# Optimization experiments

Hardware: AMD Instinct MI355X
Metric: run time of the kernel (lower is better)

## Reference

```python
import jax, jax.numpy as jnp
import numpy as np

B, T, IN, H, NC = 256, 512, 64, 512, 64
H2 = H // 2


def setup_inputs() -> dict:
    key = jax.random.key(0)
    ks = jax.random.split(key, 13)
    s = 0.05
    return {
        "x": jax.random.normal(ks[0], (B, T, IN), jnp.float32),
        # layer 0 LSTM weights (PyTorch layout: [4H, in], gate order i,f,g,o)
        "w_ih0": jax.random.normal(ks[1], (4 * H, IN), jnp.float32) * s,
        "w_hh0": jax.random.normal(ks[2], (4 * H, H), jnp.float32) * s,
        "b_ih0": jax.random.normal(ks[3], (4 * H,), jnp.float32) * s,
        "b_hh0": jax.random.normal(ks[4], (4 * H,), jnp.float32) * s,
        # layer 1 LSTM weights
        "w_ih1": jax.random.normal(ks[5], (4 * H, H), jnp.float32) * s,
        "w_hh1": jax.random.normal(ks[6], (4 * H, H), jnp.float32) * s,
        "b_ih1": jax.random.normal(ks[7], (4 * H,), jnp.float32) * s,
        "b_hh1": jax.random.normal(ks[8], (4 * H,), jnp.float32) * s,
        # classifier head
        "w1": jax.random.normal(ks[9], (H2, H), jnp.float32) * s,
        "b1": jax.random.normal(ks[10], (H2,), jnp.float32) * s,
        "w2": jax.random.normal(ks[11], (NC, H2), jnp.float32) * s,
        "b2": jax.random.normal(ks[12], (NC,), jnp.float32) * s,
    }


def _lstm_layer(x, w_ih, w_hh, b_ih, b_hh):
    # x: [B, T, D_in] -> hidden sequence [B, T, H]
    b, t, _ = x.shape
    h_dim = w_hh.shape[1]
    # precompute input projection for all time steps: [B, T, 4H]
    gx = jnp.einsum('btd,gd->btg', x, w_ih) + b_ih + b_hh

    def step(carry, g_t):
        h, c = carry
        gates = g_t + h @ w_hh.T  # [B, 4H]
        i, f, g, o = jnp.split(gates, 4, axis=-1)
        i = jax.nn.sigmoid(i)
        f = jax.nn.sigmoid(f)
        g = jnp.tanh(g)
        o = jax.nn.sigmoid(o)
        c_new = f * c + i * g
        h_new = o * jnp.tanh(c_new)
        return (h_new, c_new), h_new

    h0 = jnp.zeros((b, h_dim), x.dtype)
    c0 = jnp.zeros((b, h_dim), x.dtype)
    (_, _), hs = jax.lax.scan(step, (h0, c0), jnp.swapaxes(gx, 0, 1))
    return jnp.swapaxes(hs, 0, 1)  # [B, T, H]


def reference(x, w_ih0, w_hh0, b_ih0, b_hh0, w_ih1, w_hh1, b_ih1, b_hh1, w1, b1, w2, b2):
    # 2-layer LSTM (eval mode: inter-layer dropout disabled)
    out = _lstm_layer(x, w_ih0, w_hh0, b_ih0, b_hh0)
    out = _lstm_layer(out, w_ih1, w_hh1, b_ih1, b_hh1)
    feat = out[:, -1, :]  # last time step hidden state [B, H]
    # classifier: Linear -> ReLU -> (Dropout off in eval) -> Linear
    hmid = jax.nn.relu(feat @ w1.T + b1)
    logits = hmid @ w2.T + b2
    return logits
```

## Files before the change

### kernel.cpp

```cpp
#include <hip/hip_runtime.h>
#include <stdint.h>

#define B_  256
#define T_  512
#define IN_ 64
#define H_  512
#define G4_ 2048
#define NC_ 64
#define H2_ 256

typedef _Float16 f16;
typedef __attribute__((ext_vector_type(4))) _Float16 f16x4;
typedef __attribute__((ext_vector_type(4))) float    f32x4;
typedef __attribute__((ext_vector_type(4))) unsigned int u32x4;

__device__ __forceinline__ float sigf(float x) {
  return __builtin_amdgcn_rcpf(1.0f + __expf(-x));
}
__device__ __forceinline__ float tanh_fast(float x) {
  x = fminf(fmaxf(x, -15.f), 15.f);
  const float e = __expf(2.f * x);
  return (e - 1.f) * __builtin_amdgcn_rcpf(e + 1.f);
}

__device__ __forceinline__ void store_u32_l3(void* p, unsigned v) {
  asm volatile("global_store_dword %0, %1, off sc0 sc1" :: "v"(p), "v"(v) : "memory");
}
__device__ __forceinline__ void store_f32_l3(void* p, float v) {
  asm volatile("global_store_dword %0, %1, off sc0 sc1" :: "v"(p), "v"(v) : "memory");
}
__device__ __forceinline__ unsigned load_u32_l3(const void* p) {
  unsigned r;
  asm volatile("global_load_dword %0, %1, off sc0 sc1" : "=v"(r) : "v"(p) : "memory");
  return r;
}
__device__ __forceinline__ float load_f32_l3(const void* p) {
  float r;
  asm volatile("global_load_dword %0, %1, off sc0 sc1" : "=v"(r) : "v"(p) : "memory");
  return r;
}
__device__ __forceinline__ u32x4 load_u32x4_l3(const void* p) {
  u32x4 r;
  asm volatile("global_load_dwordx4 %0, %1, off sc0 sc1" : "=v"(r) : "v"(p) : "memory");
  return r;
}
__device__ __forceinline__ void wait_vm0() {
  asm volatile("s_waitcnt vmcnt(0)" ::: "memory");
}

__global__ void cvt_f32_f16(const float* __restrict__ s, f16* __restrict__ d, int n) {
  int i = blockIdx.x * blockDim.x + threadIdx.x;
  int st = gridDim.x * blockDim.x;
  for (; i < n; i += st) d[i] = (f16)s[i];
}

__global__ void bias_comb(const float* __restrict__ a, const float* __restrict__ b,
                          float* __restrict__ d, int n) {
  int i = blockIdx.x * blockDim.x + threadIdx.x;
  if (i < n) d[i] = a[i] + b[i];
}

__global__ __launch_bounds__(512, 2) void fused_g(
    const f16* __restrict__ x16,
    const f16* __restrict__ wih0,
    const f16* __restrict__ whh0,
    const f16* __restrict__ wih1,
    const f16* __restrict__ whh1,
    const float* __restrict__ bias0,
    const float* __restrict__ bias1,
    f16* __restrict__ h0seq,
    float* __restrict__ gxring,
    f16* __restrict__ hbuf1,
    unsigned* __restrict__ flags) {
  __shared__ __align__(16) unsigned char smem[36352];
  const int bid = blockIdx.x;
  const int tid = threadIdx.x;
  const int lane = tid & 63, wv = tid >> 6;
  const int l15 = lane & 15, hi = lane >> 4;

  if (bid < 128) {
    const int grp = bid >> 3, sl = bid & 7;
    f16 (*xt)[72]   = (f16(*)[72])smem;
    f16 (*ht)[532]  = (f16(*)[532])(smem + 2304);
    float (*gl)[260] = (float(*)[260])(smem + 2304 + 17024);

    int gidx[2]; f16x4 bhh[2][32]; f16x4 bih[2][4]; float bv[2];
#pragma unroll
    for (int nt = 0; nt < 2; ++nt) {
      const int lg = (wv * 2 + nt) * 16 + l15;
      const int grow = (lg >> 6) * H_ + sl * 64 + (lg & 63);
      gidx[nt] = grow; bv[nt] = bias0[grow];
      const f16* wp = whh0 + (size_t)grow * H_;
#pragma unroll
      for (int ks = 0; ks < 32; ++ks) bhh[nt][ks] = *(const f16x4*)(wp + ks * 16 + 4 * hi);
      const f16* wq = wih0 + (size_t)grow * IN_;
#pragma unroll
      for (int ks = 0; ks < 4; ++ks) bih[nt][ks] = *(const f16x4*)(wq + ks * 16 + 4 * hi);
    }

    const int bl = tid >> 5;
    const int j0 = (tid & 31) * 2;
    float c0 = 0.f, c1 = 0.f;
    const int hrow = tid >> 5, hcol = (tid & 31) * 16;

    for (int t = 0; t < T_; ++t) {
      if (tid < 128) {
        const f16* xs = x16 + ((size_t)(grp * 16 + (tid >> 3)) * T_ + t) * IN_ + (tid & 7) * 8;
        *(uint4*)&xt[tid >> 3][(tid & 7) * 8] = *(const uint4*)xs;
      }
      if (t != 0) {
        const unsigned* pp = flags + (size_t)(grp * 8 + (lane & 7)) * 16;
        const unsigned want = (unsigned)t;
        for (;;) {
          unsigned v = load_u32_l3(pp); wait_vm0();
          if (__all((int)(v >= want))) break;
          __builtin_amdgcn_s_sleep(1);
        }
        const f16* hs = h0seq + ((size_t)(t - 1) * B_ + grp * 16 + hrow) * H_ + hcol;
        u32x4 r0 = load_u32x4_l3(hs);
        u32x4 r1 = load_u32x4_l3(hs + 8);
        wait_vm0();
        __builtin_amdgcn_sched_barrier(0);
        *(u32x4*)&ht[hrow][hcol]     = r0;
        *(u32x4*)&ht[hrow][hcol + 8] = r1;
      } else {
        u32x4 z = {0u, 0u, 0u, 0u};
        *(u32x4*)&ht[hrow][hcol]     = z;
        *(u32x4*)&ht[hrow][hcol + 8] = z;
      }
      __syncthreads();

      f32x4 acc[2];
#pragma unroll
      for (int nt = 0; nt < 2; ++nt) { acc[nt][0] = bv[nt]; acc[nt][1] = bv[nt]; acc[nt][2] = bv[nt]; acc[nt][3] = bv[nt]; }
#pragma unroll
      for (int ks = 0; ks < 4; ++ks) {
        const f16x4 a = *(const f16x4*)&xt[l15][ks * 16 + 4 * hi];
        acc[0] = __builtin_amdgcn_mfma_f32_16x16x16f16(a, bih[0][ks], acc[0], 0, 0, 0);
        acc[1] = __builtin_amdgcn_mfma_f32_16x16x16f16(a, bih[1][ks], acc[1], 0, 0, 0);
      }
#pragma unroll
      for (int ks = 0; ks < 32; ++ks) {
        const f16x4 a = *(const f16x4*)&ht[l15][ks * 16 + 4 * hi];
        acc[0] = __builtin_amdgcn_mfma_f32_16x16x16f16(a, bhh[0][ks], acc[0], 0, 0, 0);
        acc[1] = __builtin_amdgcn_mfma_f32_16x16x16f16(a, bhh[1][ks], acc[1], 0, 0, 0);
      }
#pragma unroll
      for (int nt = 0; nt < 2; ++nt) {
        const int col = (wv * 2 + nt) * 16 + l15;
#pragma unroll
        for (int r = 0; r < 4; ++r) gl[4 * hi + r][col] = acc[nt][r];
      }
      __syncthreads();

      const float gi = gl[bl][j0],        gi1 = gl[bl][j0 + 1];
      const float gf = gl[bl][64 + j0],   gf1 = gl[bl][64 + j0 + 1];
      const float gg = gl[bl][128 + j0],  gg1 = gl[bl][128 + j0 + 1];
      const float go = gl[bl][192 + j0],  go1 = gl[bl][192 + j0 + 1];
      c0 = sigf(gf) * c0 + sigf(gi) * tanh_fast(gg);
      c1 = sigf(gf1) * c1 + sigf(gi1) * tanh_fast(gg1);
      const f16 h0h = (f16)(sigf(go) * tanh_fast(c0));
      const f16 h1h = (f16)(sigf(go1) * tanh_fast(c1));
      unsigned hp = ((unsigned)__builtin_bit_cast(unsigned short, h1h) << 16)
                  |  (unsigned)__builtin_bit_cast(unsigned short, h0h);
      store_u32_l3(h0seq + ((size_t)t * B_ + grp * 16 + bl) * H_ + sl * 64 + j0, hp);
      wait_vm0();
      __syncthreads();
      if (tid == 0) store_u32_l3(flags + (size_t)(grp * 8 + sl) * 16, (unsigned)(t + 1));
    }

  } else if (bid < 192) {
    const int bg = (bid - 128) >> 3, slB = (bid - 128) & 7;
    f16 (*ht)[532] = (f16(*)[532])smem;

    int gidx[2]; f16x4 bih[2][32]; float bv[2];
#pragma unroll
    for (int nt = 0; nt < 2; ++nt) {
      const int grow = slB * 256 + (wv * 2 + nt) * 16 + l15;
      gidx[nt] = grow; bv[nt] = bias1[grow];
      const f16* wp = wih1 + (size_t)grow * H_;
#pragma unroll
      for (int ks = 0; ks < 32; ++ks) bih[nt][ks] = *(const f16x4*)(wp + ks * 16 + 4 * hi);
    }
    const int hrow = tid >> 4, hcol = (tid & 15) * 32;

    for (int t = 0; t < T_; ++t) {
      {
        const bool isC = (lane >= 16 && lane < 24);
        const unsigned wantC = (t >= 8) ? (unsigned)(t - 7) : 0u;
        const int slot = isC ? (192 + bg * 8 + (lane - 16)) : (bg * 16 + (lane & 15));
        const unsigned want = isC ? wantC : (unsigned)(t + 1);
        const unsigned* pp = flags + (size_t)slot * 16;
        for (;;) {
          unsigned v = load_u32_l3(pp); wait_vm0();
          if (__all((int)(v >= want))) break;
          __builtin_amdgcn_s_sleep(1);
        }
      }
      {
        const f16* hs = h0seq + ((size_t)t * B_ + bg * 32 + hrow) * H_ + hcol;
        u32x4 r0 = load_u32x4_l3(hs);
        u32x4 r1 = load_u32x4_l3(hs + 8);
        u32x4 r2 = load_u32x4_l3(hs + 16);
        u32x4 r3 = load_u32x4_l3(hs + 24);
        wait_vm0();
        __builtin_amdgcn_sched_barrier(0);
        *(u32x4*)&ht[hrow][hcol]      = r0;
        *(u32x4*)&ht[hrow][hcol + 8]  = r1;
        *(u32x4*)&ht[hrow][hcol + 16] = r2;
        *(u32x4*)&ht[hrow][hcol + 24] = r3;
      }
      __syncthreads();

      f32x4 acc[2][2] = {};
#pragma unroll
      for (int ks = 0; ks < 32; ++ks) {
        const f16x4 a0 = *(const f16x4*)&ht[l15][ks * 16 + 4 * hi];
        const f16x4 a1 = *(const f16x4*)&ht[16 + l15][ks * 16 + 4 * hi];
        acc[0][0] = __builtin_amdgcn_mfma_f32_16x16x16f16(a0, bih[0][ks], acc[0][0], 0, 0, 0);
        acc[0][1] = __builtin_amdgcn_mfma_f32_16x16x16f16(a0, bih[1][ks], acc[0][1], 0, 0, 0);
        acc[1][0] = __builtin_amdgcn_mfma_f32_16x16x16f16(a1, bih[0][ks], acc[1][0], 0, 0, 0);
        acc[1][1] = __builtin_amdgcn_mfma_f32_16x16x16f16(a1, bih[1][ks], acc[1][1], 0, 0, 0);
      }
      float* gp = gxring + (size_t)(t & 7) * B_ * G4_;
#pragma unroll
      for (int mt = 0; mt < 2; ++mt)
#pragma unroll
        for (int nt = 0; nt < 2; ++nt)
#pragma unroll
          for (int r = 0; r < 4; ++r)
            store_f32_l3(gp + (size_t)(bg * 32 + mt * 16 + 4 * hi + r) * G4_ + gidx[nt],
                         acc[mt][nt][r] + bv[nt]);
      wait_vm0();
      __syncthreads();
      if (tid == 0) store_u32_l3(flags + (size_t)(128 + bg * 8 + slB) * 16, (unsigned)(t + 1));
    }

  } else {
    const int bg = (bid - 192) >> 3, slC = (bid - 192) & 7;
    f16 (*ht)[532]   = (f16(*)[532])smem;
    float (*gl)[260] = (float(*)[260])smem;

    int gidx[2]; f16x4 bhh[2][32];
#pragma unroll
    for (int nt = 0; nt < 2; ++nt) {
      const int lg = (wv * 2 + nt) * 16 + l15;
      const int grow = (lg >> 6) * H_ + slC * 64 + (lg & 63);
      gidx[nt] = grow;
      const f16* wp = whh1 + (size_t)grow * H_;
#pragma unroll
      for (int ks = 0; ks < 32; ++ks) bhh[nt][ks] = *(const f16x4*)(wp + ks * 16 + 4 * hi);
    }
    const int r0row = tid >> 5;
    const int j0 = (tid & 31) * 2;
    float c00 = 0.f, c01 = 0.f, c10 = 0.f, c11 = 0.f;
    const int hrow = tid >> 4, hcol = (tid & 15) * 32;

    for (int t = 0; t < T_; ++t) {
      {
        const bool isOwn = (lane >= 8 && lane < 16);
        const unsigned wantOwn = (t >= 1) ? (unsigned)t : 0u;
        const int slot = isOwn ? (192 + bg * 8 + (lane - 8)) : (128 + bg * 8 + (lane & 7));
        const unsigned want = isOwn ? wantOwn : (unsigned)(t + 1);
        const unsigned* pp = flags + (size_t)slot * 16;
        for (;;) {
          unsigned v = load_u32_l3(pp); wait_vm0();
          if (__all((int)(v >= want))) break;
          __builtin_amdgcn_s_sleep(1);
        }
      }
      float gxv[2][2][4];
      const float* gp = gxring + (size_t)(t & 7) * B_ * G4_;
#pragma unroll
      for (int mt = 0; mt < 2; ++mt)
#pragma unroll
        for (int nt = 0; nt < 2; ++nt)
#pragma unroll
          for (int r = 0; r < 4; ++r)
            gxv[mt][nt][r] = load_f32_l3(gp + (size_t)(bg * 32 + mt * 16 + 4 * hi + r) * G4_ + gidx[nt]);
      if (t != 0) {
        const f16* hs = hbuf1 + ((size_t)((t - 1) & 1) * B_ + bg * 32 + hrow) * H_ + hcol;
        u32x4 r0 = load_u32x4_l3(hs);
        u32x4 r1 = load_u32x4_l3(hs + 8);
        u32x4 r2 = load_u32x4_l3(hs + 16);
        u32x4 r3 = load_u32x4_l3(hs + 24);
        wait_vm0();
        __builtin_amdgcn_sched_barrier(0);
        *(u32x4*)&ht[hrow][hcol]      = r0;
        *(u32x4*)&ht[hrow][hcol + 8]  = r1;
        *(u32x4*)&ht[hrow][hcol + 16] = r2;
        *(u32x4*)&ht[hrow][hcol + 24] = r3;
      } else {
        wait_vm0();
        u32x4 z = {0u, 0u, 0u, 0u};
        *(u32x4*)&ht[hrow][hcol]      = z;
        *(u32x4*)&ht[hrow][hcol + 8]  = z;
        *(u32x4*)&ht[hrow][hcol + 16] = z;
        *(u32x4*)&ht[hrow][hcol + 24] = z;
      }
      __syncthreads();

      f32x4 acc[2][2];
#pragma unroll
      for (int mt = 0; mt < 2; ++mt)
#pragma unroll
        for (int nt = 0; nt < 2; ++nt)
#pragma unroll
          for (int r = 0; r < 4; ++r) acc[mt][nt][r] = gxv[mt][nt][r];
#pragma unroll
      for (int ks = 0; ks < 32; ++ks) {
        const f16x4 a0 = *(const f16x4*)&ht[l15][ks * 16 + 4 * hi];
        const f16x4 a1 = *(const f16x4*)&ht[16 + l15][ks * 16 + 4 * hi];
        acc[0][0] = __builtin_amdgcn_mfma_f32_16x16x16f16(a0, bhh[0][ks], acc[0][0], 0, 0, 0);
        acc[0][1] = __builtin_amdgcn_mfma_f32_16x16x16f16(a0, bhh[1][ks], acc[0][1], 0, 0, 0);
        acc[1][0] = __builtin_amdgcn_mfma_f32_16x16x16f16(a1, bhh[0][ks], acc[1][0], 0, 0, 0);
        acc[1][1] = __builtin_amdgcn_mfma_f32_16x16x16f16(a1, bhh[1][ks], acc[1][1], 0, 0, 0);
      }
      __syncthreads();
#pragma unroll
      for (int mt = 0; mt < 2; ++mt)
#pragma unroll
        for (int nt = 0; nt < 2; ++nt) {
          const int col = (wv * 2 + nt) * 16 + l15;
#pragma unroll
          for (int r = 0; r < 4; ++r) gl[mt * 16 + 4 * hi + r][col] = acc[mt][nt][r];
        }
      __syncthreads();

      const int cur = t & 1;
#pragma unroll
      for (int half = 0; half < 2; ++half) {
        const int row = r0row + half * 16;
        const float gi = gl[row][j0],        gi1 = gl[row][j0 + 1];
        const float gf = gl[row][64 + j0],   gf1 = gl[row][64 + j0 + 1];
        const float gg = gl[row][128 + j0],  gg1 = gl[row][128 + j0 + 1];
        const float go = gl[row][192 + j0],  go1 = gl[row][192 + j0 + 1];
        float& ca = half ? c10 : c00;
        float& cb = half ? c11 : c01;
        ca = sigf(gf) * ca + sigf(gi) * tanh_fast(gg);
        cb = sigf(gf1) * cb + sigf(gi1) * tanh_fast(gg1);
        const f16 ha = (f16)(sigf(go) * tanh_fast(ca));
        const f16 hb = (f16)(sigf(go1) * tanh_fast(cb));
        unsigned hp = ((unsigned)__builtin_bit_cast(unsigned short, hb) << 16)
                    |  (unsigned)__builtin_bit_cast(unsigned short, ha);
        store_u32_l3(hbuf1 + ((size_t)cur * B_ + bg * 32 + row) * H_ + slC * 64 + j0, hp);
      }
      wait_vm0();
      __syncthreads();
      if (tid == 0) store_u32_l3(flags + (size_t)(192 + bg * 8 + slC) * 16, (unsigned)(t + 1));
    }
  }
}

__global__ void head_g(const f16* __restrict__ h1, const float* __restrict__ w1,
                       const float* __restrict__ b1, const float* __restrict__ w2,
                       const float* __restrict__ b2, float* __restrict__ out) {
  __shared__ float ft[512];
  __shared__ float hm[256];
  const int b = blockIdx.x, tid = threadIdx.x;
  ft[tid * 2]     = (float)h1[(size_t)b * H_ + tid * 2];
  ft[tid * 2 + 1] = (float)h1[(size_t)b * H_ + tid * 2 + 1];
  __syncthreads();
  {
    float d = b1[tid];
    const float* wr = w1 + (size_t)tid * H_;
#pragma unroll 8
    for (int k = 0; k < H_; ++k) d += ft[k] * wr[k];
    hm[tid] = fmaxf(d, 0.f);
  }
  __syncthreads();
  if (tid < NC_) {
    float d = b2[tid];
    const float* wr = w2 + (size_t)tid * H2_;
#pragma unroll 8
    for (int k = 0; k < H2_; ++k) d += hm[k] * wr[k];
    out[(size_t)b * NC_ + tid] = d;
  }
}

extern "C" void kernel_launch(void* const* d_in, const int* in_sizes, int n_in,
                              void* d_out, int out_size, void* d_ws, size_t ws_size,
                              hipStream_t stream) {
  const float* x     = (const float*)d_in[0];
  const float* w_ih0 = (const float*)d_in[1];
  const float* w_hh0 = (const float*)d_in[2];
  const float* b_ih0 = (const float*)d_in[3];
  const float* b_hh0 = (const float*)d_in[4];
  const float* w_ih1 = (const float*)d_in[5];
  const float* w_hh1 = (const float*)d_in[6];
  const float* b_ih1 = (const float*)d_in[7];
  const float* b_hh1 = (const float*)d_in[8];
  const float* w1    = (const float*)d_in[9];
  const float* b1    = (const float*)d_in[10];
  const float* w2    = (const float*)d_in[11];
  const float* b2    = (const float*)d_in[12];
  float* out = (float*)d_out;

  char* p = (char*)d_ws;
  auto alloc = [&](size_t bytes) { char* r = p; p += (bytes + 255) & ~(size_t)255; return r; };
  f16*   h0seq  = (f16*)alloc((size_t)T_ * B_ * H_ * 2);
  float* gxring = (float*)alloc((size_t)8 * B_ * G4_ * 4);
  f16*   hbuf1  = (f16*)alloc((size_t)2 * B_ * H_ * 2);
  f16*   x16    = (f16*)alloc((size_t)B_ * T_ * IN_ * 2);
  f16*   wih0h  = (f16*)alloc((size_t)G4_ * IN_ * 2);
  f16*   whh0h  = (f16*)alloc((size_t)G4_ * H_ * 2);
  f16*   wih1h  = (f16*)alloc((size_t)G4_ * H_ * 2);
  f16*   whh1h  = (f16*)alloc((size_t)G4_ * H_ * 2);
  float* bias0c = (float*)alloc(G4_ * 4);
  float* bias1c = (float*)alloc(G4_ * 4);
  unsigned* flags = (unsigned*)alloc(256 * 64);

  hipMemsetAsync(flags, 0, 256 * 64, stream);
  cvt_f32_f16<<<2048, 256, 0, stream>>>(x, x16, B_ * T_ * IN_);
  cvt_f32_f16<<<512, 256, 0, stream>>>(w_ih0, wih0h, G4_ * IN_);
  cvt_f32_f16<<<2048, 256, 0, stream>>>(w_hh0, whh0h, G4_ * H_);
  cvt_f32_f16<<<2048, 256, 0, stream>>>(w_ih1, wih1h, G4_ * H_);
  cvt_f32_f16<<<2048, 256, 0, stream>>>(w_hh1, whh1h, G4_ * H_);
  bias_comb<<<8, 256, 0, stream>>>(b_ih0, b_hh0, bias0c, G4_);
  bias_comb<<<8, 256, 0, stream>>>(b_ih1, b_hh1, bias1c, G4_);

  fused_g<<<256, 512, 0, stream>>>(x16, wih0h, whh0h, wih1h, whh1h,
                                   bias0c, bias1c, h0seq, gxring, hbuf1, flags);
  head_g<<<B_, 256, 0, stream>>>(hbuf1 + (size_t)B_ * H_, w1, b1, w2, b2, out);
}
```

Before: 3.309 ms.

## Fuse layer-1 input projection into recurrent blocks, drop gx ring buffer

Measured after the change: 3.518 ms. 6.3% more time.

```diff
diff --git a/kernel.cpp b/kernel.cpp
--- a/kernel.cpp
+++ b/kernel.cpp
@@ -26,16 +26,8 @@
 __device__ __forceinline__ void store_u32_l3(void* p, unsigned v) {
   asm volatile("global_store_dword %0, %1, off sc0 sc1" :: "v"(p), "v"(v) : "memory");
 }
-__device__ __forceinline__ void store_f32_l3(void* p, float v) {
-  asm volatile("global_store_dword %0, %1, off sc0 sc1" :: "v"(p), "v"(v) : "memory");
-}
 __device__ __forceinline__ unsigned load_u32_l3(const void* p) {
   unsigned r;
-  asm volatile("global_load_dword %0, %1, off sc0 sc1" : "=v"(r) : "v"(p) : "memory");
-  return r;
-}
-__device__ __forceinline__ float load_f32_l3(const void* p) {
-  float r;
   asm volatile("global_load_dword %0, %1, off sc0 sc1" : "=v"(r) : "v"(p) : "memory");
   return r;
 }
@@ -69,10 +61,9 @@
     const float* __restrict__ bias0,
     const float* __restrict__ bias1,
     f16* __restrict__ h0seq,
-    float* __restrict__ gxring,
     f16* __restrict__ hbuf1,
     unsigned* __restrict__ flags) {
-  __shared__ __align__(16) unsigned char smem[36352];
+  __shared__ __align__(16) unsigned char smem[50688];
   const int bid = blockIdx.x;
   const int tid = threadIdx.x;
   const int lane = tid & 63, wv = tid >> 6;
@@ -169,27 +160,36 @@
       if (tid == 0) store_u32_l3(flags + (size_t)(grp * 8 + sl) * 16, (unsigned)(t + 1));
     }
 
-  } else if (bid < 192) {
-    const int bg = (bid - 128) >> 3, slB = (bid - 128) & 7;
-    f16 (*ht)[532] = (f16(*)[532])smem;
-
-    int gidx[2]; f16x4 bih[2][32]; float bv[2];
+  } else {
+    const int grp = (bid - 128) >> 3, sl = (bid - 128) & 7;
+    f16 (*ht0)[532]  = (f16(*)[532])smem;
+    f16 (*ht1)[532]  = (f16(*)[532])(smem + 17024);
+    float (*gl)[260] = (float(*)[260])(smem + 34048);
+
+    int gidx[2]; f16x4 bih[2][32]; f16x4 bhh[2][32]; float bv[2];
 #pragma unroll
     for (int nt = 0; nt < 2; ++nt) {
-      const int grow = slB * 256 + (wv * 2 + nt) * 16 + l15;
+      const int lg = (wv * 2 + nt) * 16 + l15;
+      const int grow = (lg >> 6) * H_ + sl * 64 + (lg & 63);
       gidx[nt] = grow; bv[nt] = bias1[grow];
       const f16* wp = wih1 + (size_t)grow * H_;
 #pragma unroll
       for (int ks = 0; ks < 32; ++ks) bih[nt][ks] = *(const f16x4*)(wp + ks * 16 + 4 * hi);
+      const f16* wq = whh1 + (size_t)grow * H_;
+#pragma unroll
+      for (int ks = 0; ks < 32; ++ks) bhh[nt][ks] = *(const f16x4*)(wq + ks * 16 + 4 * hi);
     }
-    const int hrow = tid >> 4, hcol = (tid & 15) * 32;
+
+    const int bl = tid >> 5;
+    const int j0 = (tid & 31) * 2;
+    float c0 = 0.f, c1 = 0.f;
+    const int hrow = tid >> 5, hcol = (tid & 31) * 16;
 
     for (int t = 0; t < T_; ++t) {
       {
-        const bool isC = (lane >= 16 && lane < 24);
-        const unsigned wantC = (t >= 8) ? (unsigned)(t - 7) : 0u;
-        const int slot = isC ? (192 + bg * 8 + (lane - 16)) : (bg * 16 + (lane & 15));
-        const unsigned want = isC ? wantC : (unsigned)(t + 1);
+        const bool isOwn = (lane >= 8 && lane < 16);
+        const int slot = isOwn ? (128 + grp * 8 + (lane - 8)) : (grp * 8 + (lane & 7));
+        const unsigned want = isOwn ? (unsigned)t : (unsigned)(t + 1);
         const unsigned* pp = flags + (size_t)slot * 16;
         for (;;) {
           unsigned v = load_u32_l3(pp); wait_vm0();
@@ -198,156 +198,66 @@
         }
       }
       {
-        const f16* hs = h0seq + ((size_t)t * B_ + bg * 32 + hrow) * H_ + hcol;
-        u32x4 r0 = load_u32x4_l3(hs);
-        u32x4 r1 = load_u32x4_l3(hs + 8);
-        u32x4 r2 = load_u32x4_l3(hs + 16);
-        u32x4 r3 = load_u32x4_l3(hs + 24);
-        wait_vm0();
-        __builtin_amdgcn_sched_barrier(0);
-        *(u32x4*)&ht[hrow][hcol]      = r0;
-        *(u32x4*)&ht[hrow][hcol + 8]  = r1;
-        *(u32x4*)&ht[hrow][hcol + 16] = r2;
-        *(u32x4*)&ht[hrow][hcol + 24] = r3;
-      }
-      __syncthreads();
-
-      f32x4 acc[2][2] = {};
+        const f16* hs0 = h0seq + ((size_t)t * B_ + grp * 16 + hrow) * H_ + hcol;
+        u32x4 r0 = load_u32x4_l3(hs0);
+        u32x4 r1 = load_u32x4_l3(hs0 + 8);
+        if (t != 0) {
+          const f16* hs1 = hbuf1 + ((size_t)((t - 1) & 1) * B_ + grp * 16 + hrow) * H_ + hcol;
+          u32x4 r2 = load_u32x4_l3(hs1);
+          u32x4 r3 = load_u32x4_l3(hs1 + 8);
+          wait_vm0();
+          __builtin_amdgcn_sched_barrier(0);
+          *(u32x4*)&ht1[hrow][hcol]     = r2;
+          *(u32x4*)&ht1[hrow][hcol + 8] = r3;
+        } else {
+          wait_vm0();
+          __builtin_amdgcn_sched_barrier(0);
+          u32x4 z = {0u, 0u, 0u, 0u};
+          *(u32x4*)&ht1[hrow][hcol]     = z;
+          *(u32x4*)&ht1[hrow][hcol + 8] = z;
+        }
+        *(u32x4*)&ht0[hrow][hcol]     = r0;
+        *(u32x4*)&ht0[hrow][hcol + 8] = r1;
+      }
+      __syncthreads();
+
+      f32x4 acc[2];
+#pragma unroll
+      for (int nt = 0; nt < 2; ++nt) { acc[nt][0] = bv[nt]; acc[nt][1] = bv[nt]; acc[nt][2] = bv[nt]; acc[nt][3] = bv[nt]; }
 #pragma unroll
       for (int ks = 0; ks < 32; ++ks) {
-        const f16x4 a0 = *(const f16x4*)&ht[l15][ks * 16 + 4 * hi];
-        const f16x4 a1 = *(const f16x4*)&ht[16 + l15][ks * 16 + 4 * hi];
-        acc[0][0] = __builtin_amdgcn_mfma_f32_16x16x16f16(a0, bih[0][ks], acc[0][0], 0, 0, 0);
-        acc[0][1] = __builtin_amdgcn_mfma_f32_16x16x16f16(a0, bih[1][ks], acc[0][1], 0, 0, 0);
-        acc[1][0] = __builtin_amdgcn_mfma_f32_16x16x16f16(a1, bih[0][ks], acc[1][0], 0, 0, 0);
-        acc[1][1] = __builtin_amdgcn_mfma_f32_16x16x16f16(a1, bih[1][ks], acc[1][1], 0, 0, 0);
-      }
-      float* gp = gxring + (size_t)(t & 7) * B_ * G4_;
-#pragma unroll
-      for (int mt = 0; mt < 2; ++mt)
-#pragma unroll
-        for (int nt = 0; nt < 2; ++nt)
-#pragma unroll
-          for (int r = 0; r < 4; ++r)
-            store_f32_l3(gp + (size_t)(bg * 32 + mt * 16 + 4 * hi + r) * G4_ + gidx[nt],
-                         acc[mt][nt][r] + bv[nt]);
+        const f16x4 a0 = *(const f16x4*)&ht0[l15][ks * 16 + 4 * hi];
+        acc[0] = __builtin_amdgcn_mfma_f32_16x16x16f16(a0, bih[0][ks], acc[0], 0, 0, 0);
+        acc[1] = __builtin_amdgcn_mfma_f32_16x16x16f16(a0, bih[1][ks], acc[1], 0, 0, 0);
+      }
+#pragma unroll
+      for (int ks = 0; ks < 32; ++ks) {
+        const f16x4 a1 = *(const f16x4*)&ht1[l15][ks * 16 + 4 * hi];
+        acc[0] = __builtin_amdgcn_mfma_f32_16x16x16f16(a1, bhh[0][ks], acc[0], 0, 0, 0);
+        acc[1] = __builtin_amdgcn_mfma_f32_16x16x16f16(a1, bhh[1][ks], acc[1], 0, 0, 0);
+      }
+#pragma unroll
+      for (int nt = 0; nt < 2; ++nt) {
+        const int col = (wv * 2 + nt) * 16 + l15;
+#pragma unroll
+        for (int r = 0; r < 4; ++r) gl[4 * hi + r][col] = acc[nt][r];
+      }
+      __syncthreads();
+
+      const float gi = gl[bl][j0],        gi1 = gl[bl][j0 + 1];
+      const float gf = gl[bl][64 + j0],   gf1 = gl[bl][64 + j0 + 1];
+      const float gg = gl[bl][128 + j0],  gg1 = gl[bl][128 + j0 + 1];
+      const float go = gl[bl][192 + j0],  go1 = gl[bl][192 + j0 + 1];
+      c0 = sigf(gf) * c0 + sigf(gi) * tanh_fast(gg);
+      c1 = sigf(gf1) * c1 + sigf(gi1) * tanh_fast(gg1);
+      const f16 ha = (f16)(sigf(go) * tanh_fast(c0));
+      const f16 hb = (f16)(sigf(go1) * tanh_fast(c1));
+      unsigned hp = ((unsigned)__builtin_bit_cast(unsigned short, hb) << 16)
+                  |  (unsigned)__builtin_bit_cast(unsigned short, ha);
+      store_u32_l3(hbuf1 + ((size_t)(t & 1) * B_ + grp * 16 + bl) * H_ + sl * 64 + j0, hp);
       wait_vm0();
       __syncthreads();
-      if (tid == 0) store_u32_l3(flags + (size_t)(128 + bg * 8 + slB) * 16, (unsigned)(t + 1));
-    }
-
-  } else {
-    const int bg = (bid - 192) >> 3, slC = (bid - 192) & 7;
-    f16 (*ht)[532]   = (f16(*)[532])smem;
-    float (*gl)[260] = (float(*)[260])smem;
-
-    int gidx[2]; f16x4 bhh[2][32];
-#pragma unroll
-    for (int nt = 0; nt < 2; ++nt) {
-      const int lg = (wv * 2 + nt) * 16 + l15;
-      const int grow = (lg >> 6) * H_ + slC * 64 + (lg & 63);
-      gidx[nt] = grow;
-      const f16* wp = whh1 + (size_t)grow * H_;
-#pragma unroll
-      for (int ks = 0; ks < 32; ++ks) bhh[nt][ks] = *(const f16x4*)(wp + ks * 16 + 4 * hi);
-    }
-    const int r0row = tid >> 5;
-    const int j0 = (tid & 31) * 2;
-    float c00 = 0.f, c01 = 0.f, c10 = 0.f, c11 = 0.f;
-    const int hrow = tid >> 4, hcol = (tid & 15) * 32;
-
-    for (int t = 0; t < T_; ++t) {
-      {
-        const bool isOwn = (lane >= 8 && lane < 16);
-        const unsigned wantOwn = (t >= 1) ? (unsigned)t : 0u;
-        const int slot = isOwn ? (192 + bg * 8 + (lane - 8)) : (128 + bg * 8 + (lane & 7));
-        const unsigned want = isOwn ? wantOwn : (unsigned)(t + 1);
-        const unsigned* pp = flags + (size_t)slot * 16;
-        for (;;) {
-          unsigned v = load_u32_l3(pp); wait_vm0();
-          if (__all((int)(v >= want))) break;
-          __builtin_amdgcn_s_sleep(1);
-        }
-      }
-      float gxv[2][2][4];
-      const float* gp = gxring + (size_t)(t & 7) * B_ * G4_;
-#pragma unroll
-      for (int mt = 0; mt < 2; ++mt)
-#pragma unroll
-        for (int nt = 0; nt < 2; ++nt)
-#pragma unroll
-          for (int r = 0; r < 4; ++r)
-            gxv[mt][nt][r] = load_f32_l3(gp + (size_t)(bg * 32 + mt * 16 + 4 * hi + r) * G4_ + gidx[nt]);
-      if (t != 0) {
-        const f16* hs = hbuf1 + ((size_t)((t - 1) & 1) * B_ + bg * 32 + hrow) * H_ + hcol;
-        u32x4 r0 = load_u32x4_l3(hs);
-        u32x4 r1 = load_u32x4_l3(hs + 8);
-        u32x4 r2 = load_u32x4_l3(hs + 16);
-        u32x4 r3 = load_u32x4_l3(hs + 24);
-        wait_vm0();
-        __builtin_amdgcn_sched_barrier(0);
-        *(u32x4*)&ht[hrow][hcol]      = r0;
-        *(u32x4*)&ht[hrow][hcol + 8]  = r1;
-        *(u32x4*)&ht[hrow][hcol + 16] = r2;
-        *(u32x4*)&ht[hrow][hcol + 24] = r3;
-      } else {
-        wait_vm0();
-        u32x4 z = {0u, 0u, 0u, 0u};
-        *(u32x4*)&ht[hrow][hcol]      = z;
-        *(u32x4*)&ht[hrow][hcol + 8]  = z;
-        *(u32x4*)&ht[hrow][hcol + 16] = z;
-        *(u32x4*)&ht[hrow][hcol + 24] = z;
-      }
-      __syncthreads();
-
-      f32x4 acc[2][2];
-#pragma unroll
-      for (int mt = 0; mt < 2; ++mt)
-#pragma unroll
-        for (int nt = 0; nt < 2; ++nt)
-#pragma unroll
-          for (int r = 0; r < 4; ++r) acc[mt][nt][r] = gxv[mt][nt][r];
-#pragma unroll
-      for (int ks = 0; ks < 32; ++ks) {
-        const f16x4 a0 = *(const f16x4*)&ht[l15][ks * 16 + 4 * hi];
-        const f16x4 a1 = *(const f16x4*)&ht[16 + l15][ks * 16 + 4 * hi];
-        acc[0][0] = __builtin_amdgcn_mfma_f32_16x16x16f16(a0, bhh[0][ks], acc[0][0], 0, 0, 0);
-        acc[0][1] = __builtin_amdgcn_mfma_f32_16x16x16f16(a0, bhh[1][ks], acc[0][1], 0, 0, 0);
-        acc[1][0] = __builtin_amdgcn_mfma_f32_16x16x16f16(a1, bhh[0][ks], acc[1][0], 0, 0, 0);
-        acc[1][1] = __builtin_amdgcn_mfma_f32_16x16x16f16(a1, bhh[1][ks], acc[1][1], 0, 0, 0);
-      }
-      __syncthreads();
-#pragma unroll
-      for (int mt = 0; mt < 2; ++mt)
-#pragma unroll
-        for (int nt = 0; nt < 2; ++nt) {
-          const int col = (wv * 2 + nt) * 16 + l15;
-#pragma unroll
-          for (int r = 0; r < 4; ++r) gl[mt * 16 + 4 * hi + r][col] = acc[mt][nt][r];
-        }
-      __syncthreads();
-
-      const int cur = t & 1;
-#pragma unroll
-      for (int half = 0; half < 2; ++half) {
-        const int row = r0row + half * 16;
-        const float gi = gl[row][j0],        gi1 = gl[row][j0 + 1];
-        const float gf = gl[row][64 + j0],   gf1 = gl[row][64 + j0 + 1];
-        const float gg = gl[row][128 + j0],  gg1 = gl[row][128 + j0 + 1];
-        const float go = gl[row][192 + j0],  go1 = gl[row][192 + j0 + 1];
-        float& ca = half ? c10 : c00;
-        float& cb = half ? c11 : c01;
-        ca = sigf(gf) * ca + sigf(gi) * tanh_fast(gg);
-        cb = sigf(gf1) * cb + sigf(gi1) * tanh_fast(gg1);
-        const f16 ha = (f16)(sigf(go) * tanh_fast(ca));
-        const f16 hb = (f16)(sigf(go1) * tanh_fast(cb));
-        unsigned hp = ((unsigned)__builtin_bit_cast(unsigned short, hb) << 16)
-                    |  (unsigned)__builtin_bit_cast(unsigned short, ha);
-        store_u32_l3(hbuf1 + ((size_t)cur * B_ + bg * 32 + row) * H_ + slC * 64 + j0, hp);
-      }
-      wait_vm0();
-      __syncthreads();
-      if (tid == 0) store_u32_l3(flags + (size_t)(192 + bg * 8 + slC) * 16, (unsigned)(t + 1));
+      if (tid == 0) store_u32_l3(flags + (size_t)(128 + grp * 8 + sl) * 16, (unsigned)(t + 1));
     }
   }
 }
@@ -399,7 +309,6 @@
   char* p = (char*)d_ws;
   auto alloc = [&](size_t bytes) { char* r = p; p += (bytes + 255) & ~(size_t)255; return r; };
   f16*   h0seq  = (f16*)alloc((size_t)T_ * B_ * H_ * 2);
-  float* gxring = (float*)alloc((size_t)8 * B_ * G4_ * 4);
   f16*   hbuf1  = (f16*)alloc((size_t)2 * B_ * H_ * 2);
   f16*   x16    = (f16*)alloc((size_t)B_ * T_ * IN_ * 2);
   f16*   wih0h  = (f16*)alloc((size_t)G4_ * IN_ * 2);
@@ -420,6 +329,6 @@
   bias_comb<<<8, 256, 0, stream>>>(b_ih1, b_hh1, bias1c, G4_);
 
   fused_g<<<256, 512, 0, stream>>>(x16, wih0h, whh0h, wih1h, whh1h,
-                                   bias0c, bias1c, h0seq, gxring, hbuf1, flags);
+                                   bias0c, bias1c, h0seq, hbuf1, flags);
   head_g<<<B_, 256, 0, stream>>>(hbuf1 + (size_t)B_ * H_, w1, b1, w2, b2, out);
 }
```

## Store layer-1 input-gate ring in fp16, transposed, with deeper ring

Applied to the files above, without the earlier changes.

Result: slower. 3.480 ms (+5.2%).

```diff
diff --git a/kernel.cpp b/kernel.cpp
--- a/kernel.cpp
+++ b/kernel.cpp
@@ -12,6 +12,7 @@
 typedef _Float16 f16;
 typedef __attribute__((ext_vector_type(4))) _Float16 f16x4;
 typedef __attribute__((ext_vector_type(4))) float    f32x4;
+typedef __attribute__((ext_vector_type(2))) unsigned int u32x2;
 typedef __attribute__((ext_vector_type(4))) unsigned int u32x4;
 
 __device__ __forceinline__ float sigf(float x) {
@@ -22,21 +23,31 @@
   const float e = __expf(2.f * x);
   return (e - 1.f) * __builtin_amdgcn_rcpf(e + 1.f);
 }
+__device__ __forceinline__ unsigned pack2(float a, float b) {
+  return ((unsigned)__builtin_bit_cast(unsigned short, (f16)b) << 16)
+       |  (unsigned)__builtin_bit_cast(unsigned short, (f16)a);
+}
+__device__ __forceinline__ float unpk_lo(unsigned u) {
+  return (float)__builtin_bit_cast(f16, (unsigned short)(u & 0xffffu));
+}
+__device__ __forceinline__ float unpk_hi(unsigned u) {
+  return (float)__builtin_bit_cast(f16, (unsigned short)(u >> 16));
+}
 
 __device__ __forceinline__ void store_u32_l3(void* p, unsigned v) {
   asm volatile("global_store_dword %0, %1, off sc0 sc1" :: "v"(p), "v"(v) : "memory");
 }
-__device__ __forceinline__ void store_f32_l3(void* p, float v) {
-  asm volatile("global_store_dword %0, %1, off sc0 sc1" :: "v"(p), "v"(v) : "memory");
+__device__ __forceinline__ void store_u32x2_l3(void* p, u32x2 v) {
+  asm volatile("global_store_dwordx2 %0, %1, off sc0 sc1" :: "v"(p), "v"(v) : "memory");
 }
 __device__ __forceinline__ unsigned load_u32_l3(const void* p) {
   unsigned r;
   asm volatile("global_load_dword %0, %1, off sc0 sc1" : "=v"(r) : "v"(p) : "memory");
   return r;
 }
-__device__ __forceinline__ float load_f32_l3(const void* p) {
-  float r;
-  asm volatile("global_load_dword %0, %1, off sc0 sc1" : "=v"(r) : "v"(p) : "memory");
+__device__ __forceinline__ u32x2 load_u32x2_l3(const void* p) {
+  u32x2 r;
+  asm volatile("global_load_dwordx2 %0, %1, off sc0 sc1" : "=v"(r) : "v"(p) : "memory");
   return r;
 }
 __device__ __forceinline__ u32x4 load_u32x4_l3(const void* p) {
@@ -69,7 +80,7 @@
     const float* __restrict__ bias0,
     const float* __restrict__ bias1,
     f16* __restrict__ h0seq,
-    float* __restrict__ gxring,
+    f16* __restrict__ gxring,
     f16* __restrict__ hbuf1,
     unsigned* __restrict__ flags) {
   __shared__ __align__(16) unsigned char smem[36352];
@@ -187,7 +198,7 @@
     for (int t = 0; t < T_; ++t) {
       {
         const bool isC = (lane >= 16 && lane < 24);
-        const unsigned wantC = (t >= 8) ? (unsigned)(t - 7) : 0u;
+        const unsigned wantC = (t >= 16) ? (unsigned)(t - 15) : 0u;
         const int slot = isC ? (192 + bg * 8 + (lane - 16)) : (bg * 16 + (lane & 15));
         const unsigned want = isC ? wantC : (unsigned)(t + 1);
         const unsigned* pp = flags + (size_t)slot * 16;
@@ -222,15 +233,16 @@
         acc[1][0] = __builtin_amdgcn_mfma_f32_16x16x16f16(a1, bih[0][ks], acc[1][0], 0, 0, 0);
         acc[1][1] = __builtin_amdgcn_mfma_f32_16x16x16f16(a1, bih[1][ks], acc[1][1], 0, 0, 0);
       }
-      float* gp = gxring + (size_t)(t & 7) * B_ * G4_;
+      f16* gp = gxring + (size_t)(t & 15) * G4_ * B_;
 #pragma unroll
       for (int mt = 0; mt < 2; ++mt)
 #pragma unroll
-        for (int nt = 0; nt < 2; ++nt)
-#pragma unroll
-          for (int r = 0; r < 4; ++r)
-            store_f32_l3(gp + (size_t)(bg * 32 + mt * 16 + 4 * hi + r) * G4_ + gidx[nt],
-                         acc[mt][nt][r] + bv[nt]);
+        for (int nt = 0; nt < 2; ++nt) {
+          u32x2 pay;
+          pay.x = pack2(acc[mt][nt][0] + bv[nt], acc[mt][nt][1] + bv[nt]);
+          pay.y = pack2(acc[mt][nt][2] + bv[nt], acc[mt][nt][3] + bv[nt]);
+          store_u32x2_l3(gp + (size_t)gidx[nt] * B_ + bg * 32 + mt * 16 + 4 * hi, pay);
+        }
       wait_vm0();
       __syncthreads();
       if (tid == 0) store_u32_l3(flags + (size_t)(128 + bg * 8 + slB) * 16, (unsigned)(t + 1));
@@ -269,15 +281,13 @@
           __builtin_amdgcn_s_sleep(1);
         }
       }
-      float gxv[2][2][4];
-      const float* gp = gxring + (size_t)(t & 7) * B_ * G4_;
+      u32x2 gxv[2][2];
+      const f16* gp = gxring + (size_t)(t & 15) * G4_ * B_;
 #pragma unroll
       for (int mt = 0; mt < 2; ++mt)
 #pragma unroll
         for (int nt = 0; nt < 2; ++nt)
-#pragma unroll
-          for (int r = 0; r < 4; ++r)
-            gxv[mt][nt][r] = load_f32_l3(gp + (size_t)(bg * 32 + mt * 16 + 4 * hi + r) * G4_ + gidx[nt]);
+          gxv[mt][nt] = load_u32x2_l3(gp + (size_t)gidx[nt] * B_ + bg * 32 + mt * 16 + 4 * hi);
       if (t != 0) {
         const f16* hs = hbuf1 + ((size_t)((t - 1) & 1) * B_ + bg * 32 + hrow) * H_ + hcol;
         u32x4 r0 = load_u32x4_l3(hs);
@@ -304,9 +314,13 @@
 #pragma unroll
       for (int mt = 0; mt < 2; ++mt)
 #pragma unroll
-        for (int nt = 0; nt < 2; ++nt)
-#pragma unroll
-          for (int r = 0; r < 4; ++r) acc[mt][nt][r] = gxv[mt][nt][r];
+        for (int nt = 0; nt < 2; ++nt) {
+          const unsigned ux = gxv[mt][nt].x, uy = gxv[mt][nt].y;
+          const float v0 = unpk_lo(ux), v1 = unpk_hi(ux);
+          const float v2 = unpk_lo(uy), v3 = unpk_hi(uy);
+          acc[mt][nt][0] = v0; acc[mt][nt][1] = v1;
+          acc[mt][nt][2] = v2; acc[mt][nt][3] = v3;
+        }
 #pragma unroll
       for (int ks = 0; ks < 32; ++ks) {
         const f16x4 a0 = *(const f16x4*)&ht[l15][ks * 16 + 4 * hi];
@@ -399,7 +413,7 @@
   char* p = (char*)d_ws;
   auto alloc = [&](size_t bytes) { char* r = p; p += (bytes + 255) & ~(size_t)255; return r; };
   f16*   h0seq  = (f16*)alloc((size_t)T_ * B_ * H_ * 2);
-  float* gxring = (float*)alloc((size_t)8 * B_ * G4_ * 4);
+  f16*   gxring = (f16*)alloc((size_t)16 * G4_ * B_ * 2);
   f16*   hbuf1  = (f16*)alloc((size_t)2 * B_ * H_ * 2);
   f16*   x16    = (f16*)alloc((size_t)B_ * T_ * IN_ * 2);
   f16*   wih0h  = (f16*)alloc((size_t)G4_ * IN_ * 2);
```
